# Optimization experiments

Measured on AMD Instinct MI355X. Metric: run time of the kernel, lower is better.

Reference implementation:

```python
import jax, jax.numpy as jnp
import numpy as np

B, S, D, H, L, V = 2, 1024, 512, 8, 4, 32000
DK = D // H
EPS = 1e-6


def _positional_encoding():
    # row i of the original (d_model, seq) array: sin if i even else cos of t/10000^(2i/D); transposed -> (S, D)
    i = jnp.arange(D, dtype=jnp.float32)
    ang = jnp.arange(S, dtype=jnp.float32)[:, None] / (10000.0 ** (2.0 * i / D))[None, :]
    return jnp.where((jnp.arange(D) % 2 == 0)[None, :], jnp.sin(ang), jnp.cos(ang))


def _layernorm(x, g, b):
    m = jnp.mean(x, axis=-1, keepdims=True)
    s = jnp.std(x, axis=-1, keepdims=True)
    return g / (s + EPS) * (x - m) + b


def _mha(x, wq, wk, wv, wo, mask):
    # wq/wk/wv: [H, D, DK]; all heads batched via einsum (equivalent to per-head loop + concat)
    q = jnp.einsum('bsd,hdk->bhsk', x, wq)
    k = jnp.einsum('bsd,hdk->bhsk', x, wk)
    v = jnp.einsum('bsd,hdk->bhsk', x, wv)
    scores = jnp.einsum('bhsk,bhtk->bhst', q, k) / np.float32(np.sqrt(DK))
    if mask is not None:
        scores = scores + mask  # additive upper-tri 1e-15, faithful to source
    attn = jax.nn.softmax(scores, axis=-1)
    o = jnp.einsum('bhst,bhtv->bhsv', attn, v)
    o = o.transpose(0, 2, 1, 3).reshape(B, S, D)  # concat heads
    return o @ wo


def setup_inputs() -> dict:
    key = jax.random.key(0)
    ks = jax.random.split(key, 13)
    n = lambda k, shape, s=0.05: jax.random.normal(k, shape, dtype=jnp.float32) * s
    return {
        'tokens': jax.random.randint(ks[0], (B, S), 0, V),
        'emb': n(ks[1], (V, D)),
        'Wq': n(ks[2], (L, 2, H, D, DK)),
        'Wk': n(ks[3], (L, 2, H, D, DK)),
        'Wv': n(ks[4], (L, 2, H, D, DK)),
        'Wo': n(ks[5], (L, 2, D, D)),
        'ln_gain': 1.0 + n(ks[6], (L, 3, S, D)),
        'ln_bias': n(ks[7], (L, 3, S, D)),
        'ffn_w1': n(ks[8], (L, D, D)),
        'ffn_b1': n(ks[9], (L, D)),
        'ffn_w2': n(ks[10], (L, D, D)),
        'ffn_b2': n(ks[11], (L, D)),
    }


def reference(tokens, emb, Wq, Wk, Wv, Wo, ln_gain, ln_bias, ffn_w1, ffn_b1, ffn_w2, ffn_b2):
    pe = _positional_encoding()
    # NOTE: source applies sqrt(d_model) scalar AFTER adding positional encoding
    x = (emb[tokens] + pe[None, :, :]) * np.float32(np.sqrt(D))
    # source 'mask' adds 1e-15 to strictly-upper triangle (effectively a no-op; kept faithful)
    mask = (jnp.triu(jnp.ones((S, S), dtype=jnp.float32), 1) * 1e-15)[None, None, :, :]
    for l in range(L):
        h = _mha(x, Wq[l, 0], Wk[l, 0], Wv[l, 0], Wo[l, 0], mask)
        x = _layernorm(x + h, ln_gain[l, 0], ln_bias[l, 0])
        h = _mha(x, Wq[l, 1], Wk[l, 1], Wv[l, 1], Wo[l, 1], None)
        x = _layernorm(x + h, ln_gain[l, 1], ln_bias[l, 1])
        h = jax.nn.relu(x @ ffn_w1[l] + ffn_b1[l]) @ ffn_w2[l] + ffn_b2[l]
        x = _layernorm(x + h, ln_gain[l, 2], ln_bias[l, 2])
    # tied output projection with softmax (SharedWeights on transposed embedding)
    return jax.nn.softmax(x @ emb.T, axis=-1)
```

## Files before the change

kernel.cpp:

```cpp
#include <hip/hip_runtime.h>
#include <hip/hip_bf16.h>

typedef unsigned short u16;
typedef short bf16x8 __attribute__((ext_vector_type(8)));
typedef float f32x4 __attribute__((ext_vector_type(4)));
typedef unsigned short u16x8 __attribute__((ext_vector_type(8)));

constexpr int kB = 2;
constexpr int kS = 1024;
constexpr int kD = 512;
constexpr int kH = 8;
constexpr int kDK = 64;
constexpr int kL = 4;
constexpr int kV = 32000;
constexpr int kM = kB * kS;
constexpr int kNB = kV / 128;

__device__ __forceinline__ u16 f2bh(float x) {
  unsigned u = __builtin_bit_cast(unsigned, x);
  unsigned r = u + 0x7fffu + ((u >> 16) & 1u);
  return (u16)(r >> 16);
}
__device__ __forceinline__ float bh2f(u16 h) {
  return __builtin_bit_cast(float, (unsigned)h << 16);
}
__device__ __forceinline__ void gload16(const u16* g, u16* l) {
  __builtin_amdgcn_global_load_lds(
      (const __attribute__((address_space(1))) unsigned int*)g,
      (__attribute__((address_space(3))) unsigned int*)l, 16, 0, 0);
}
__device__ __forceinline__ size_t swz_idx(int row, int k) {
  return (size_t)row * kD + (k & ~63) + ((((k >> 3) & 7) ^ (row & 7)) << 3) + (k & 7);
}

__global__ __launch_bounds__(256)
void conv_qkv(const float* __restrict__ Wq, const float* __restrict__ Wk,
              const float* __restrict__ Wv, u16* __restrict__ oh, u16* __restrict__ ol) {
  __shared__ float ld[64][65];
  const int kc = blockIdx.x, h = blockIdx.y, z = blockIdx.z;
  const int mat = z >> 3, lj = z & 7;
  const float* src = (mat == 0 ? Wq : mat == 1 ? Wk : Wv) +
                     ((size_t)(lj * kH + h)) * kD * kDK + (size_t)kc * 64 * kDK;
  const int t = threadIdx.x;
#pragma unroll
  for (int i = 0; i < 16; ++i) {
    const int idx = i * 256 + t;
    ld[idx >> 6][idx & 63] = src[idx];
  }
  __syncthreads();
  const int dkr = t >> 2, jb = t & 3;
  const size_t rowbase = ((size_t)lj * 1536 + mat * kD + h * kDK + dkr) * kD + kc * 64;
#pragma unroll
  for (int q = 0; q < 2; ++q) {
    const int jj = jb + q * 4;
    const int jsw = jj ^ (dkr & 7);
    u16x8 hi, lo;
#pragma unroll
    for (int e = 0; e < 8; ++e) {
      float v = ld[jj * 8 + e][dkr];
      hi[e] = f2bh(v);
      lo[e] = f2bh(v - bh2f(hi[e]));
    }
    *(u16x8*)&oh[rowbase + jsw * 8] = hi;
    *(u16x8*)&ol[rowbase + jsw * 8] = lo;
  }
}

__global__ __launch_bounds__(256)
void conv_sq(const float* __restrict__ Wo, const float* __restrict__ w1,
             const float* __restrict__ w2, u16* __restrict__ woh, u16* __restrict__ wol,
             u16* __restrict__ w1h, u16* __restrict__ w1l,
             u16* __restrict__ w2h, u16* __restrict__ w2l) {
  __shared__ float ld[64][65];
  const int kc = blockIdx.x, nc = blockIdx.y, mid = blockIdx.z;
  const float* src;
  u16 *dh, *dl;
  if (mid < 8) { src = Wo + (size_t)mid * kD * kD; dh = woh + (size_t)mid * kD * kD; dl = wol + (size_t)mid * kD * kD; }
  else if (mid < 12) { int l = mid - 8; src = w1 + (size_t)l * kD * kD; dh = w1h + (size_t)l * kD * kD; dl = w1l + (size_t)l * kD * kD; }
  else { int l = mid - 12; src = w2 + (size_t)l * kD * kD; dh = w2h + (size_t)l * kD * kD; dl = w2l + (size_t)l * kD * kD; }
  const int t = threadIdx.x;
#pragma unroll
  for (int i = 0; i < 16; ++i) {
    const int idx = i * 256 + t;
    const int kl = idx >> 6, nl = idx & 63;
    ld[kl][nl] = src[(size_t)(kc * 64 + kl) * kD + nc * 64 + nl];
  }
  __syncthreads();
  const int nr = t >> 2, jb = t & 3;
  const size_t rowbase = (size_t)(nc * 64 + nr) * kD + kc * 64;
#pragma unroll
  for (int q = 0; q < 2; ++q) {
    const int jj = jb + q * 4;
    const int jsw = jj ^ (nr & 7);
    u16x8 hi, lo;
#pragma unroll
    for (int e = 0; e < 8; ++e) {
      float v = ld[jj * 8 + e][nr];
      hi[e] = f2bh(v);
      lo[e] = f2bh(v - bh2f(hi[e]));
    }
    *(u16x8*)&dh[rowbase + jsw * 8] = hi;
    *(u16x8*)&dl[rowbase + jsw * 8] = lo;
  }
}

__global__ __launch_bounds__(256)
void conv_emb(const float* __restrict__ emb, u16* __restrict__ oh) {
  const int chunk = blockIdx.x * 256 + threadIdx.x;
  const int n = chunk >> 6, j = chunk & 63;
  const float* s = &emb[(size_t)n * kD + j * 8];
  float4 a = *(const float4*)s, b = *(const float4*)(s + 4);
  u16x8 hi;
  hi[0] = f2bh(a.x); hi[1] = f2bh(a.y); hi[2] = f2bh(a.z); hi[3] = f2bh(a.w);
  hi[4] = f2bh(b.x); hi[5] = f2bh(b.y); hi[6] = f2bh(b.z); hi[7] = f2bh(b.w);
  *(u16x8*)&oh[(size_t)n * kD + (j & ~7) * 8 + (((j & 7) ^ (n & 7)) << 3)] = hi;
}

__global__ __launch_bounds__(256)
void embed_kernel(const int* __restrict__ tokens, const float* __restrict__ emb,
                  float* __restrict__ x, u16* __restrict__ xh, u16* __restrict__ xl) {
  const int row = blockIdx.x;
  const int s = row & (kS - 1);
  const int tok = tokens[row];
  const float scl = sqrtf((float)kD);
  for (int d = threadIdx.x; d < kD; d += 256) {
    float e = emb[(size_t)tok * kD + d];
    float den = powf(10000.0f, 2.0f * (float)d / (float)kD);
    float ang = (float)s / den;
    float pe = ((d & 1) == 0) ? sinf(ang) : cosf(ang);
    float o = (e + pe) * scl;
    x[(size_t)row * kD + d] = o;
    u16 hi = f2bh(o);
    size_t p = swz_idx(row, d);
    xh[p] = hi;
    xl[p] = f2bh(o - bh2f(hi));
  }
}

template <int SPLIT, int BM, int BN, int OUT, int BIAS, int RELU>
__global__ __launch_bounds__(256)
void mgemm2(const u16* __restrict__ Ah, const u16* __restrict__ Al,
            const u16* __restrict__ Bh, const u16* __restrict__ Bl,
            float* __restrict__ Cf, u16* __restrict__ Ch, u16* __restrict__ Cl,
            const float* __restrict__ bias, float* __restrict__ partials,
            int Kd, int Nd) {
  static_assert(BM == BN, "");
  constexpr int MF = BM / 32, NF = BN / 32;
  constexpr int TA = BM * 64;
  constexpr int NT = (SPLIT == 3 ? 4 : 2);
  constexpr int BUF = NT * TA;
  __shared__ __align__(16) u16 lds[2 * BUF];
  __shared__ float plds[OUT == 3 ? 2 * BM : 1];
  const int t = threadIdx.x;
  const int lane = t & 63, g = lane >> 4, li = lane & 15;
  const int w = t >> 6, wr = w >> 1, wc = w & 1;
  const int m0 = blockIdx.x * BM, n0 = blockIdx.y * BN;

  f32x4 acc[MF][NF];
#pragma unroll
  for (int i = 0; i < MF; ++i)
#pragma unroll
    for (int j = 0; j < NF; ++j) acc[i][j] = (f32x4){0.f, 0.f, 0.f, 0.f};

  auto stage = [&](int c, int k0) {
    u16* base = &lds[c * BUF];
#pragma unroll
    for (int it = 0; it < BM / 32; ++it) {
      const int idx = it * 256 + t;
      const int r = idx >> 3, j = (idx & 7) * 8;
      gload16(&Ah[(size_t)(m0 + r) * Kd + k0 + j], &base[idx * 8]);
      if (SPLIT == 3)
        gload16(&Al[(size_t)(m0 + r) * Kd + k0 + j], &base[TA + idx * 8]);
      gload16(&Bh[(size_t)(n0 + r) * Kd + k0 + j],
              &base[(SPLIT == 3 ? 2 : 1) * TA + idx * 8]);
      if (SPLIT == 3)
        gload16(&Bl[(size_t)(n0 + r) * Kd + k0 + j], &base[3 * TA + idx * 8]);
    }
  };
  auto compute = [&](int c) {
    const u16* base = &lds[c * BUF];
#pragma unroll
    for (int s = 0; s < 2; ++s) {
      const int s4g = s * 4 + g;
      bf16x8 fah[MF], fbh[NF], fal[SPLIT == 3 ? MF : 1], fbl[SPLIT == 3 ? NF : 1];
#pragma unroll
      for (int fm = 0; fm < MF; ++fm) {
        const int row = wr * (BM / 2) + fm * 16 + li;
        const int off = row * 64 + ((s4g ^ (row & 7)) << 3);
        fah[fm] = *(const bf16x8*)&base[off];
        if (SPLIT == 3) fal[fm] = *(const bf16x8*)&base[TA + off];
      }
#pragma unroll
      for (int fn = 0; fn < NF; ++fn) {
        const int row = wc * (BN / 2) + fn * 16 + li;
        const int off = row * 64 + ((s4g ^ (row & 7)) << 3);
        fbh[fn] = *(const bf16x8*)&base[(SPLIT == 3 ? 2 : 1) * TA + off];
        if (SPLIT == 3) fbl[fn] = *(const bf16x8*)&base[3 * TA + off];
      }
#pragma unroll
      for (int fm = 0; fm < MF; ++fm)
#pragma unroll
        for (int fn = 0; fn < NF; ++fn) {
          acc[fm][fn] = __builtin_amdgcn_mfma_f32_16x16x32_bf16(
              fah[fm], fbh[fn], acc[fm][fn], 0, 0, 0);
          if (SPLIT == 3) {
            acc[fm][fn] = __builtin_amdgcn_mfma_f32_16x16x32_bf16(
                fal[fm], fbh[fn], acc[fm][fn], 0, 0, 0);
            acc[fm][fn] = __builtin_amdgcn_mfma_f32_16x16x32_bf16(
                fah[fm], fbl[fn], acc[fm][fn], 0, 0, 0);
          }
        }
    }
  };

  stage(0, 0);
  __syncthreads();
  int cur = 0;
  for (int k0 = 64; k0 < Kd; k0 += 64) {
    stage(cur ^ 1, k0);
    compute(cur);
    __syncthreads();
    cur ^= 1;
  }
  compute(cur);

#pragma unroll
  for (int fm = 0; fm < MF; ++fm)
#pragma unroll
    for (int fn = 0; fn < NF; ++fn)
#pragma unroll
      for (int r = 0; r < 4; ++r) {
        const int m = m0 + wr * (BM / 2) + fm * 16 + g * 4 + r;
        const int n = n0 + wc * (BN / 2) + fn * 16 + li;
        float c = acc[fm][fn][r];
        if (BIAS) c += bias[n];
        if (RELU) c = fmaxf(c, 0.0f);
        if (OUT == 0) {
          Cf[(size_t)m * Nd + n] = c;
        } else if (OUT == 1) {
          u16 hi = f2bh(c);
          size_t p = swz_idx(m, n);
          Ch[p] = hi;
          Cl[p] = f2bh(c - bh2f(hi));
        } else if (OUT == 2) {
          const int mat = n >> 9, h = (n >> 6) & 7, dk = n & 63;
          const int b_ = m >> 10, s_ = m & (kS - 1);
          Ch[(size_t)mat * ((size_t)kM * kDK * kH / 8) * 8 +
             (((size_t)(b_ * kH + h) * kS + s_) * kDK + dk)] = f2bh(c);
        } else {
          u16 q = f2bh(__expf(c));
          Ch[(size_t)m * Nd + n] = q;
          acc[fm][fn][r] = bh2f(q);
        }
      }
  if (OUT == 3) {
#pragma unroll
    for (int fm = 0; fm < MF; ++fm)
#pragma unroll
      for (int r = 0; r < 4; ++r) {
        float sv = 0.f;
#pragma unroll
        for (int fn = 0; fn < NF; ++fn) sv += acc[fm][fn][r];
        sv += __shfl_xor(sv, 1); sv += __shfl_xor(sv, 2);
        sv += __shfl_xor(sv, 4); sv += __shfl_xor(sv, 8);
        if (li == 0) plds[wc * BM + wr * (BM / 2) + fm * 16 + g * 4 + r] = sv;
      }
    __syncthreads();
    if (t < BM)
      partials[(size_t)(m0 + t) * gridDim.y + blockIdx.y] = plds[t] + plds[BM + t];
  }
}

__global__ __launch_bounds__(256)
void attn_kernel(const u16* __restrict__ qg, const u16* __restrict__ kg,
                 const u16* __restrict__ vg, u16* __restrict__ aoh,
                 u16* __restrict__ aol) {
  __shared__ __align__(16) u16 Kt[2][64][40];
  __shared__ __align__(16) u16 Vt[2][64][40];
  __shared__ __align__(16) u16 Pt[2][64][40];
  const int t = threadIdx.x;
  const int lane = t & 63;
  const int g = lane >> 4, li = lane & 15;
  const int w = t >> 6;
  const int bh = blockIdx.y;
  const int q0 = blockIdx.x * 64;
  const size_t base = (size_t)bh * kS * kDK;
  {
    const int r = t >> 2, dq = (t & 3) * 16;
    const u16* src = &qg[base + (size_t)(q0 + r) * kDK + dq];
    u16x8 a = *(const u16x8*)src;
    u16x8 b = *(const u16x8*)(src + 8);
    *(u16x8*)&Kt[dq >> 5][r][dq & 31] = a;
    *(u16x8*)&Kt[dq >> 5][r][(dq & 31) + 8] = b;
  }
  __syncthreads();
  bf16x8 qf0 = *(const bf16x8*)&Kt[0][w * 16 + li][g * 8];
  bf16x8 qf1 = *(const bf16x8*)&Kt[1][w * 16 + li][g * 8];

  float m_[4] = {-1e30f, -1e30f, -1e30f, -1e30f};
  float l_[4] = {0.f, 0.f, 0.f, 0.f};
  f32x4 apv[4];
#pragma unroll
  for (int i = 0; i < 4; ++i) apv[i] = (f32x4){0.f, 0.f, 0.f, 0.f};

  for (int kt = 0; kt < kS / 64; ++kt) {
    __syncthreads();
    {
      const int r = t >> 2, dq = (t & 3) * 16;
      const u16* ks = &kg[base + (size_t)(kt * 64 + r) * kDK + dq];
      u16x8 a = *(const u16x8*)ks;
      u16x8 b = *(const u16x8*)(ks + 8);
      *(u16x8*)&Kt[dq >> 5][r][dq & 31] = a;
      *(u16x8*)&Kt[dq >> 5][r][(dq & 31) + 8] = b;
      const u16* vs = &vg[base + (size_t)(kt * 64 + r) * kDK + dq];
      u16x8 va = *(const u16x8*)vs;
      u16x8 vb = *(const u16x8*)(vs + 8);
      const int vc = r >> 5, ko = (r & 31) >> 3, kp = r & 7;
#pragma unroll
      for (int i = 0; i < 8; ++i) {
        const int d = dq + i;
        Vt[vc][d][((ko ^ (d >> 4)) << 3) | kp] = va[i];
      }
#pragma unroll
      for (int i = 0; i < 8; ++i) {
        const int d = dq + 8 + i;
        Vt[vc][d][((ko ^ (d >> 4)) << 3) | kp] = vb[i];
      }
    }
    __syncthreads();
    f32x4 s[4];
#pragma unroll
    for (int nf = 0; nf < 4; ++nf) {
      bf16x8 k0 = *(const bf16x8*)&Kt[0][nf * 16 + li][g * 8];
      bf16x8 k1 = *(const bf16x8*)&Kt[1][nf * 16 + li][g * 8];
      f32x4 sa = (f32x4){0.f, 0.f, 0.f, 0.f};
      sa = __builtin_amdgcn_mfma_f32_16x16x32_bf16(qf0, k0, sa, 0, 0, 0);
      sa = __builtin_amdgcn_mfma_f32_16x16x32_bf16(qf1, k1, sa, 0, 0, 0);
      s[nf] = sa;
    }
    float corr[4];
#pragma unroll
    for (int r = 0; r < 4; ++r) {
      float tm = fmaxf(fmaxf(s[0][r], s[1][r]), fmaxf(s[2][r], s[3][r])) * 0.125f;
      tm = fmaxf(tm, __shfl_xor(tm, 1));
      tm = fmaxf(tm, __shfl_xor(tm, 2));
      tm = fmaxf(tm, __shfl_xor(tm, 4));
      tm = fmaxf(tm, __shfl_xor(tm, 8));
      const float nm = fmaxf(m_[r], tm);
      corr[r] = __expf(m_[r] - nm);
      m_[r] = nm;
    }
    float tsum[4] = {0.f, 0.f, 0.f, 0.f};
    u16 pb[4][4];
#pragma unroll
    for (int nf = 0; nf < 4; ++nf)
#pragma unroll
      for (int r = 0; r < 4; ++r) {
        float p = __expf(s[nf][r] * 0.125f - m_[r]);
        tsum[r] += p;
        pb[nf][r] = f2bh(p);
      }
#pragma unroll
    for (int r = 0; r < 4; ++r) {
      float ts = tsum[r];
      ts += __shfl_xor(ts, 1); ts += __shfl_xor(ts, 2);
      ts += __shfl_xor(ts, 4); ts += __shfl_xor(ts, 8);
      l_[r] = l_[r] * corr[r] + ts;
#pragma unroll
      for (int nf = 0; nf < 4; ++nf) apv[nf][r] *= corr[r];
    }
#pragma unroll
    for (int nf = 0; nf < 4; ++nf)
#pragma unroll
      for (int r = 0; r < 4; ++r)
        Pt[nf >> 1][w * 16 + g * 4 + r][(nf & 1) * 16 + li] = pb[nf][r];
    bf16x8 p0 = *(const bf16x8*)&Pt[0][w * 16 + li][g * 8];
    bf16x8 p1 = *(const bf16x8*)&Pt[1][w * 16 + li][g * 8];
#pragma unroll
    for (int nf = 0; nf < 4; ++nf) {
      bf16x8 v0 = *(const bf16x8*)&Vt[0][nf * 16 + li][((g ^ nf) & 3) * 8];
      bf16x8 v1 = *(const bf16x8*)&Vt[1][nf * 16 + li][((g ^ nf) & 3) * 8];
      apv[nf] = __builtin_amdgcn_mfma_f32_16x16x32_bf16(p0, v0, apv[nf], 0, 0, 0);
      apv[nf] = __builtin_amdgcn_mfma_f32_16x16x32_bf16(p1, v1, apv[nf], 0, 0, 0);
    }
  }
  const int b_ = bh >> 3, h_ = bh & 7;
#pragma unroll
  for (int r = 0; r < 4; ++r) {
    const float inv = 1.0f / l_[r];
    const int row = q0 + w * 16 + g * 4 + r;
    const int m = b_ * kS + row;
#pragma unroll
    for (int nf = 0; nf < 4; ++nf) {
      const int d = h_ * kDK + nf * 16 + li;
      float o = apv[nf][r] * inv;
      u16 hi = f2bh(o);
      size_t p = swz_idx(m, d);
      aoh[p] = hi;
      aol[p] = f2bh(o - bh2f(hi));
    }
  }
}

__global__ __launch_bounds__(256)
void ln_kernel(float* __restrict__ x, const float* __restrict__ h,
               const float* __restrict__ gain, const float* __restrict__ bias,
               u16* __restrict__ xh, u16* __restrict__ xl) {
  const int row = blockIdx.x;
  const int s = row & (kS - 1);
  const int t = threadIdx.x;
  float* xr = x + (size_t)row * kD;
  const float* hr = h + (size_t)row * kD;
  const float v0 = xr[t] + hr[t];
  const float v1 = xr[t + 256] + hr[t + 256];
  float sum = v0 + v1;
  float sq = v0 * v0 + v1 * v1;
#pragma unroll
  for (int off = 1; off < 64; off <<= 1) {
    sum += __shfl_xor(sum, off);
    sq += __shfl_xor(sq, off);
  }
  __shared__ float rs[4], rq[4];
  if ((t & 63) == 0) { rs[t >> 6] = sum; rq[t >> 6] = sq; }
  __syncthreads();
  sum = rs[0] + rs[1] + rs[2] + rs[3];
  sq = rq[0] + rq[1] + rq[2] + rq[3];
  const float mean = sum * (1.0f / kD);
  const float var = fmaxf(sq * (1.0f / kD) - mean * mean, 0.0f);
  const float inv = 1.0f / (sqrtf(var) + 1e-6f);
  const float* gr = gain + (size_t)s * kD;
  const float* br = bias + (size_t)s * kD;
  const float o0 = gr[t] * inv * (v0 - mean) + br[t];
  const float o1 = gr[t + 256] * inv * (v1 - mean) + br[t + 256];
  xr[t] = o0;
  xr[t + 256] = o1;
  {
    u16 hi = f2bh(o0);
    size_t p = swz_idx(row, t);
    xh[p] = hi; xl[p] = f2bh(o0 - bh2f(hi));
  }
  {
    u16 hi = f2bh(o1);
    size_t p = swz_idx(row, t + 256);
    xh[p] = hi; xl[p] = f2bh(o1 - bh2f(hi));
  }
}

__global__ __launch_bounds__(256)
void scale_kernel(const u16* __restrict__ expb, const float* __restrict__ partials,
                  float* __restrict__ out) {
  const int row = blockIdx.x;
  const int t = threadIdx.x;
  float s = (t < kNB) ? partials[(size_t)row * kNB + t] : 0.f;
#pragma unroll
  for (int off = 1; off < 64; off <<= 1) s += __shfl_xor(s, off);
  __shared__ float red[4];
  if ((t & 63) == 0) red[t >> 6] = s;
  __syncthreads();
  const float inv = 1.0f / (red[0] + red[1] + red[2] + red[3]);
  const u16x8* src = (const u16x8*)(expb + (size_t)row * kV);
  float4* dst = (float4*)(out + (size_t)row * kV);
  for (int i = t; i < kV / 8; i += 256) {
    u16x8 v = src[i];
    float4 a = make_float4(bh2f(v[0]) * inv, bh2f(v[1]) * inv,
                           bh2f(v[2]) * inv, bh2f(v[3]) * inv);
    float4 b = make_float4(bh2f(v[4]) * inv, bh2f(v[5]) * inv,
                           bh2f(v[6]) * inv, bh2f(v[7]) * inv);
    dst[i * 2] = a;
    dst[i * 2 + 1] = b;
  }
}

extern "C" void kernel_launch(void* const* d_in, const int* in_sizes, int n_in,
                              void* d_out, int out_size, void* d_ws, size_t ws_size,
                              hipStream_t stream) {
  (void)in_sizes; (void)n_in; (void)out_size; (void)ws_size;
  const int* tokens = (const int*)d_in[0];
  const float* emb = (const float*)d_in[1];
  const float* Wq = (const float*)d_in[2];
  const float* Wk = (const float*)d_in[3];
  const float* Wv = (const float*)d_in[4];
  const float* Wo = (const float*)d_in[5];
  const float* lng = (const float*)d_in[6];
  const float* lnb = (const float*)d_in[7];
  const float* w1 = (const float*)d_in[8];
  const float* b1 = (const float*)d_in[9];
  const float* w2 = (const float*)d_in[10];
  const float* b2 = (const float*)d_in[11];

  size_t off = 0;
  auto alloc = [&](size_t bytes) {
    void* p = (char*)d_ws + off;
    off += (bytes + 255) & ~(size_t)255;
    return p;
  };
  const size_t NA = (size_t)kM * kD;
  float* x = (float*)alloc(NA * 4);
  u16* xh = (u16*)alloc(NA * 2);
  u16* xl = (u16*)alloc(NA * 2);
  u16* qkvb = (u16*)alloc(3 * NA * 2);
  u16* aoh = (u16*)alloc(NA * 2);
  u16* aol = (u16*)alloc(NA * 2);
  float* t1 = (float*)alloc(NA * 4);
  u16* t1h = (u16*)alloc(NA * 2);
  u16* t1l = (u16*)alloc(NA * 2);
  float* ao2 = (float*)alloc(NA * 4);
  float* partials = (float*)alloc((size_t)kM * kNB * 4);
  u16* expb = (u16*)alloc((size_t)kM * kV * 2);
  u16* wqkvh = (u16*)alloc((size_t)8 * 1536 * kD * 2);
  u16* wqkvl = (u16*)alloc((size_t)8 * 1536 * kD * 2);
  u16* woh = (u16*)alloc((size_t)8 * kD * kD * 2);
  u16* wol = (u16*)alloc((size_t)8 * kD * kD * 2);
  u16* w1h = (u16*)alloc((size_t)4 * kD * kD * 2);
  u16* w1l = (u16*)alloc((size_t)4 * kD * kD * 2);
  u16* w2h = (u16*)alloc((size_t)4 * kD * kD * 2);
  u16* w2l = (u16*)alloc((size_t)4 * kD * kD * 2);
  u16* embh = (u16*)alloc((size_t)kV * kD * 2);

  conv_qkv<<<dim3(8, 8, 24), 256, 0, stream>>>(Wq, Wk, Wv, wqkvh, wqkvl);
  conv_sq<<<dim3(8, 8, 16), 256, 0, stream>>>(Wo, w1, w2, woh, wol, w1h, w1l, w2h, w2l);
  conv_emb<<<kV * kD / 8 / 256, 256, 0, stream>>>(emb, embh);
  embed_kernel<<<kM, 256, 0, stream>>>(tokens, emb, x, xh, xl);

  for (int l = 0; l < kL; ++l) {
    for (int j = 0; j < 2; ++j) {
      const size_t lj = (size_t)(l * 2 + j);
      mgemm2<3, 128, 128, 2, 0, 0><<<dim3(kM / 128, 12), 256, 0, stream>>>(
          xh, xl, wqkvh + lj * 1536 * kD, wqkvl + lj * 1536 * kD,
          nullptr, qkvb, nullptr, nullptr, nullptr, kD, 1536);
      attn_kernel<<<dim3(kS / 64, kB * kH), 256, 0, stream>>>(
          qkvb, qkvb + NA, qkvb + 2 * NA, aoh, aol);
      mgemm2<3, 64, 64, 0, 0, 0><<<dim3(kM / 64, kD / 64), 256, 0, stream>>>(
          aoh, aol, woh + lj * kD * kD, wol + lj * kD * kD,
          t1, nullptr, nullptr, nullptr, nullptr, kD, kD);
      ln_kernel<<<kM, 256, 0, stream>>>(x, t1, lng + (size_t)(l * 3 + j) * kS * kD,
                                        lnb + (size_t)(l * 3 + j) * kS * kD, xh, xl);
    }
    mgemm2<3, 64, 64, 1, 1, 1><<<dim3(kM / 64, kD / 64), 256, 0, stream>>>(
        xh, xl, w1h + (size_t)l * kD * kD, w1l + (size_t)l * kD * kD,
        nullptr, t1h, t1l, b1 + (size_t)l * kD, nullptr, kD, kD);
    mgemm2<3, 64, 64, 0, 1, 0><<<dim3(kM / 64, kD / 64), 256, 0, stream>>>(
        t1h, t1l, w2h + (size_t)l * kD * kD, w2l + (size_t)l * kD * kD,
        ao2, nullptr, nullptr, b2 + (size_t)l * kD, nullptr, kD, kD);
    ln_kernel<<<kM, 256, 0, stream>>>(x, ao2, lng + (size_t)(l * 3 + 2) * kS * kD,
                                      lnb + (size_t)(l * 3 + 2) * kS * kD, xh, xl);
  }
  mgemm2<1, 128, 128, 3, 0, 0><<<dim3(kM / 128, kNB), 256, 0, stream>>>(
      xh, nullptr, embh, nullptr, nullptr, expb, nullptr, nullptr, partials,
      kD, kV);
  scale_kernel<<<kM, 256, 0, stream>>>(expb, partials, (float*)d_out);
}
```

Measured before the change: 823.0 us.

## Replace split-bf16 three-pass GEMMs with single-pass fp16 and double-buffer attention K/V

Every layer GEMM previously split operands into bf16 hi/lo pairs and issued three MFMAs per tile to emulate fp32 accuracy. This switches all operands to a single fp16 representation with one MFMA per tile, which drops the lo buffers and cuts MFMA work and memory traffic roughly threefold. The attention kernel also moves to fp16 and double-buffers K/V tiles in LDS, prefetching the next tile into registers during compute. The cost is lower precision: fp16 has a narrower range, which is risky for activations scaled by sqrt(D), and the output error grows.

```diff
diff --git a/kernel.cpp b/kernel.cpp
--- a/kernel.cpp
+++ b/kernel.cpp
@@ -2,7 +2,7 @@
 #include <hip/hip_bf16.h>
 
 typedef unsigned short u16;
-typedef short bf16x8 __attribute__((ext_vector_type(8)));
+typedef _Float16 f16x8 __attribute__((ext_vector_type(8)));
 typedef float f32x4 __attribute__((ext_vector_type(4)));
 typedef unsigned short u16x8 __attribute__((ext_vector_type(8)));
 
@@ -16,6 +16,13 @@
 constexpr int kM = kB * kS;
 constexpr int kNB = kV / 128;
 
+__device__ __forceinline__ u16 f2fh(float x) {
+  _Float16 h = (_Float16)x;
+  return __builtin_bit_cast(u16, h);
+}
+__device__ __forceinline__ float fh2f(u16 h) {
+  return (float)__builtin_bit_cast(_Float16, h);
+}
 __device__ __forceinline__ u16 f2bh(float x) {
   unsigned u = __builtin_bit_cast(unsigned, x);
   unsigned r = u + 0x7fffu + ((u >> 16) & 1u);
@@ -35,7 +42,7 @@
 
 __global__ __launch_bounds__(256)
 void conv_qkv(const float* __restrict__ Wq, const float* __restrict__ Wk,
-              const float* __restrict__ Wv, u16* __restrict__ oh, u16* __restrict__ ol) {
+              const float* __restrict__ Wv, u16* __restrict__ oh) {
   __shared__ float ld[64][65];
   const int kc = blockIdx.x, h = blockIdx.y, z = blockIdx.z;
   const int mat = z >> 3, lj = z & 7;
@@ -54,30 +61,24 @@
   for (int q = 0; q < 2; ++q) {
     const int jj = jb + q * 4;
     const int jsw = jj ^ (dkr & 7);
-    u16x8 hi, lo;
-#pragma unroll
-    for (int e = 0; e < 8; ++e) {
-      float v = ld[jj * 8 + e][dkr];
-      hi[e] = f2bh(v);
-      lo[e] = f2bh(v - bh2f(hi[e]));
-    }
+    u16x8 hi;
+#pragma unroll
+    for (int e = 0; e < 8; ++e) hi[e] = f2fh(ld[jj * 8 + e][dkr]);
     *(u16x8*)&oh[rowbase + jsw * 8] = hi;
-    *(u16x8*)&ol[rowbase + jsw * 8] = lo;
   }
 }
 
 __global__ __launch_bounds__(256)
 void conv_sq(const float* __restrict__ Wo, const float* __restrict__ w1,
-             const float* __restrict__ w2, u16* __restrict__ woh, u16* __restrict__ wol,
-             u16* __restrict__ w1h, u16* __restrict__ w1l,
-             u16* __restrict__ w2h, u16* __restrict__ w2l) {
+             const float* __restrict__ w2, u16* __restrict__ woh,
+             u16* __restrict__ w1h, u16* __restrict__ w2h) {
   __shared__ float ld[64][65];
   const int kc = blockIdx.x, nc = blockIdx.y, mid = blockIdx.z;
   const float* src;
-  u16 *dh, *dl;
-  if (mid < 8) { src = Wo + (size_t)mid * kD * kD; dh = woh + (size_t)mid * kD * kD; dl = wol + (size_t)mid * kD * kD; }
-  else if (mid < 12) { int l = mid - 8; src = w1 + (size_t)l * kD * kD; dh = w1h + (size_t)l * kD * kD; dl = w1l + (size_t)l * kD * kD; }
-  else { int l = mid - 12; src = w2 + (size_t)l * kD * kD; dh = w2h + (size_t)l * kD * kD; dl = w2l + (size_t)l * kD * kD; }
+  u16* dh;
+  if (mid < 8) { src = Wo + (size_t)mid * kD * kD; dh = woh + (size_t)mid * kD * kD; }
+  else if (mid < 12) { int l = mid - 8; src = w1 + (size_t)l * kD * kD; dh = w1h + (size_t)l * kD * kD; }
+  else { int l = mid - 12; src = w2 + (size_t)l * kD * kD; dh = w2h + (size_t)l * kD * kD; }
   const int t = threadIdx.x;
 #pragma unroll
   for (int i = 0; i < 16; ++i) {
@@ -92,15 +93,10 @@
   for (int q = 0; q < 2; ++q) {
     const int jj = jb + q * 4;
     const int jsw = jj ^ (nr & 7);
-    u16x8 hi, lo;
-#pragma unroll
-    for (int e = 0; e < 8; ++e) {
-      float v = ld[jj * 8 + e][nr];
-      hi[e] = f2bh(v);
-      lo[e] = f2bh(v - bh2f(hi[e]));
-    }
+    u16x8 hi;
+#pragma unroll
+    for (int e = 0; e < 8; ++e) hi[e] = f2fh(ld[jj * 8 + e][nr]);
     *(u16x8*)&dh[rowbase + jsw * 8] = hi;
-    *(u16x8*)&dl[rowbase + jsw * 8] = lo;
   }
 }
 
@@ -111,14 +107,14 @@
   const float* s = &emb[(size_t)n * kD + j * 8];
   float4 a = *(const float4*)s, b = *(const float4*)(s + 4);
   u16x8 hi;
-  hi[0] = f2bh(a.x); hi[1] = f2bh(a.y); hi[2] = f2bh(a.z); hi[3] = f2bh(a.w);
-  hi[4] = f2bh(b.x); hi[5] = f2bh(b.y); hi[6] = f2bh(b.z); hi[7] = f2bh(b.w);
+  hi[0] = f2fh(a.x); hi[1] = f2fh(a.y); hi[2] = f2fh(a.z); hi[3] = f2fh(a.w);
+  hi[4] = f2fh(b.x); hi[5] = f2fh(b.y); hi[6] = f2fh(b.z); hi[7] = f2fh(b.w);
   *(u16x8*)&oh[(size_t)n * kD + (j & ~7) * 8 + (((j & 7) ^ (n & 7)) << 3)] = hi;
 }
 
 __global__ __launch_bounds__(256)
 void embed_kernel(const int* __restrict__ tokens, const float* __restrict__ emb,
-                  float* __restrict__ x, u16* __restrict__ xh, u16* __restrict__ xl) {
+                  float* __restrict__ x, u16* __restrict__ xh) {
   const int row = blockIdx.x;
   const int s = row & (kS - 1);
   const int tok = tokens[row];
@@ -130,25 +126,20 @@
     float pe = ((d & 1) == 0) ? sinf(ang) : cosf(ang);
     float o = (e + pe) * scl;
     x[(size_t)row * kD + d] = o;
-    u16 hi = f2bh(o);
-    size_t p = swz_idx(row, d);
-    xh[p] = hi;
-    xl[p] = f2bh(o - bh2f(hi));
-  }
-}
-
-template <int SPLIT, int BM, int BN, int OUT, int BIAS, int RELU>
-__global__ __launch_bounds__(256)
-void mgemm2(const u16* __restrict__ Ah, const u16* __restrict__ Al,
-            const u16* __restrict__ Bh, const u16* __restrict__ Bl,
-            float* __restrict__ Cf, u16* __restrict__ Ch, u16* __restrict__ Cl,
+    xh[swz_idx(row, d)] = f2fh(o);
+  }
+}
+
+template <int BM, int BN, int OUT, int BIAS, int RELU>
+__global__ __launch_bounds__(256)
+void mgemm2(const u16* __restrict__ Ah, const u16* __restrict__ Bh,
+            float* __restrict__ Cf, u16* __restrict__ Ch,
             const float* __restrict__ bias, float* __restrict__ partials,
             int Kd, int Nd) {
   static_assert(BM == BN, "");
   constexpr int MF = BM / 32, NF = BN / 32;
   constexpr int TA = BM * 64;
-  constexpr int NT = (SPLIT == 3 ? 4 : 2);
-  constexpr int BUF = NT * TA;
+  constexpr int BUF = 2 * TA;
   __shared__ __align__(16) u16 lds[2 * BUF];
   __shared__ float plds[OUT == 3 ? 2 * BM : 1];
   const int t = threadIdx.x;
@@ -169,12 +160,7 @@
       const int idx = it * 256 + t;
       const int r = idx >> 3, j = (idx & 7) * 8;
       gload16(&Ah[(size_t)(m0 + r) * Kd + k0 + j], &base[idx * 8]);
-      if (SPLIT == 3)
-        gload16(&Al[(size_t)(m0 + r) * Kd + k0 + j], &base[TA + idx * 8]);
-      gload16(&Bh[(size_t)(n0 + r) * Kd + k0 + j],
-              &base[(SPLIT == 3 ? 2 : 1) * TA + idx * 8]);
-      if (SPLIT == 3)
-        gload16(&Bl[(size_t)(n0 + r) * Kd + k0 + j], &base[3 * TA + idx * 8]);
+      gload16(&Bh[(size_t)(n0 + r) * Kd + k0 + j], &base[TA + idx * 8]);
     }
   };
   auto compute = [&](int c) {
@@ -182,34 +168,23 @@
 #pragma unroll
     for (int s = 0; s < 2; ++s) {
       const int s4g = s * 4 + g;
-      bf16x8 fah[MF], fbh[NF], fal[SPLIT == 3 ? MF : 1], fbl[SPLIT == 3 ? NF : 1];
+      f16x8 fah[MF], fbh[NF];
 #pragma unroll
       for (int fm = 0; fm < MF; ++fm) {
         const int row = wr * (BM / 2) + fm * 16 + li;
-        const int off = row * 64 + ((s4g ^ (row & 7)) << 3);
-        fah[fm] = *(const bf16x8*)&base[off];
-        if (SPLIT == 3) fal[fm] = *(const bf16x8*)&base[TA + off];
+        fah[fm] = *(const f16x8*)&base[row * 64 + ((s4g ^ (row & 7)) << 3)];
       }
 #pragma unroll
       for (int fn = 0; fn < NF; ++fn) {
         const int row = wc * (BN / 2) + fn * 16 + li;
-        const int off = row * 64 + ((s4g ^ (row & 7)) << 3);
-        fbh[fn] = *(const bf16x8*)&base[(SPLIT == 3 ? 2 : 1) * TA + off];
-        if (SPLIT == 3) fbl[fn] = *(const bf16x8*)&base[3 * TA + off];
+        fbh[fn] = *(const f16x8*)&base[TA + row * 64 + ((s4g ^ (row & 7)) << 3)];
       }
 #pragma unroll
       for (int fm = 0; fm < MF; ++fm)
 #pragma unroll
-        for (int fn = 0; fn < NF; ++fn) {
-          acc[fm][fn] = __builtin_amdgcn_mfma_f32_16x16x32_bf16(
+        for (int fn = 0; fn < NF; ++fn)
+          acc[fm][fn] = __builtin_amdgcn_mfma_f32_16x16x32_f16(
               fah[fm], fbh[fn], acc[fm][fn], 0, 0, 0);
-          if (SPLIT == 3) {
-            acc[fm][fn] = __builtin_amdgcn_mfma_f32_16x16x32_bf16(
-                fal[fm], fbh[fn], acc[fm][fn], 0, 0, 0);
-            acc[fm][fn] = __builtin_amdgcn_mfma_f32_16x16x32_bf16(
-                fah[fm], fbl[fn], acc[fm][fn], 0, 0, 0);
-          }
-        }
     }
   };
 
@@ -238,15 +213,12 @@
         if (OUT == 0) {
           Cf[(size_t)m * Nd + n] = c;
         } else if (OUT == 1) {
-          u16 hi = f2bh(c);
-          size_t p = swz_idx(m, n);
-          Ch[p] = hi;
-          Cl[p] = f2bh(c - bh2f(hi));
+          Ch[swz_idx(m, n)] = f2fh(c);
         } else if (OUT == 2) {
           const int mat = n >> 9, h = (n >> 6) & 7, dk = n & 63;
           const int b_ = m >> 10, s_ = m & (kS - 1);
-          Ch[(size_t)mat * ((size_t)kM * kDK * kH / 8) * 8 +
-             (((size_t)(b_ * kH + h) * kS + s_) * kDK + dk)] = f2bh(c);
+          Ch[((size_t)mat * kM) * kD +
+             (((size_t)(b_ * kH + h) * kS + s_) * kDK + dk)] = f2fh(c);
         } else {
           u16 q = f2bh(__expf(c));
           Ch[(size_t)m * Nd + n] = q;
@@ -273,10 +245,9 @@
 
 __global__ __launch_bounds__(256)
 void attn_kernel(const u16* __restrict__ qg, const u16* __restrict__ kg,
-                 const u16* __restrict__ vg, u16* __restrict__ aoh,
-                 u16* __restrict__ aol) {
-  __shared__ __align__(16) u16 Kt[2][64][40];
-  __shared__ __align__(16) u16 Vt[2][64][40];
+                 const u16* __restrict__ vg, u16* __restrict__ aoh) {
+  __shared__ __align__(16) u16 Kt[2][2][64][40];
+  __shared__ __align__(16) u16 Vt[2][2][64][40];
   __shared__ __align__(16) u16 Pt[2][64][40];
   const int t = threadIdx.x;
   const int lane = t & 63;
@@ -285,17 +256,19 @@
   const int bh = blockIdx.y;
   const int q0 = blockIdx.x * 64;
   const size_t base = (size_t)bh * kS * kDK;
+  const int r = t >> 2, dq = (t & 3) * 16;
+
   {
-    const int r = t >> 2, dq = (t & 3) * 16;
     const u16* src = &qg[base + (size_t)(q0 + r) * kDK + dq];
     u16x8 a = *(const u16x8*)src;
     u16x8 b = *(const u16x8*)(src + 8);
-    *(u16x8*)&Kt[dq >> 5][r][dq & 31] = a;
-    *(u16x8*)&Kt[dq >> 5][r][(dq & 31) + 8] = b;
-  }
-  __syncthreads();
-  bf16x8 qf0 = *(const bf16x8*)&Kt[0][w * 16 + li][g * 8];
-  bf16x8 qf1 = *(const bf16x8*)&Kt[1][w * 16 + li][g * 8];
+    *(u16x8*)&Pt[dq >> 5][r][dq & 31] = a;
+    *(u16x8*)&Pt[dq >> 5][r][(dq & 31) + 8] = b;
+  }
+  __syncthreads();
+  f16x8 qf0 = *(const f16x8*)&Pt[0][w * 16 + li][g * 8];
+  f16x8 qf1 = *(const f16x8*)&Pt[1][w * 16 + li][g * 8];
+  __syncthreads();
 
   float m_[4] = {-1e30f, -1e30f, -1e30f, -1e30f};
   float l_[4] = {0.f, 0.f, 0.f, 0.f};
@@ -303,101 +276,104 @@
 #pragma unroll
   for (int i = 0; i < 4; ++i) apv[i] = (f32x4){0.f, 0.f, 0.f, 0.f};
 
+  u16x8 ka, kb, va, vb;
+  auto load_tile = [&](int kt) {
+    const u16* ks = &kg[base + (size_t)(kt * 64 + r) * kDK + dq];
+    ka = *(const u16x8*)ks;
+    kb = *(const u16x8*)(ks + 8);
+    const u16* vs = &vg[base + (size_t)(kt * 64 + r) * kDK + dq];
+    va = *(const u16x8*)vs;
+    vb = *(const u16x8*)(vs + 8);
+  };
+  auto store_tile = [&](int c) {
+    *(u16x8*)&Kt[c][dq >> 5][r][dq & 31] = ka;
+    *(u16x8*)&Kt[c][dq >> 5][r][(dq & 31) + 8] = kb;
+    const int vc = r >> 5, ko = (r & 31) >> 3, kp = r & 7;
+#pragma unroll
+    for (int i = 0; i < 8; ++i) {
+      const int d = dq + i;
+      Vt[c][vc][d][((ko ^ (d >> 4)) << 3) | kp] = va[i];
+    }
+#pragma unroll
+    for (int i = 0; i < 8; ++i) {
+      const int d = dq + 8 + i;
+      Vt[c][vc][d][((ko ^ (d >> 4)) << 3) | kp] = vb[i];
+    }
+  };
+
+  load_tile(0);
+  store_tile(0);
   for (int kt = 0; kt < kS / 64; ++kt) {
-    __syncthreads();
-    {
-      const int r = t >> 2, dq = (t & 3) * 16;
-      const u16* ks = &kg[base + (size_t)(kt * 64 + r) * kDK + dq];
-      u16x8 a = *(const u16x8*)ks;
-      u16x8 b = *(const u16x8*)(ks + 8);
-      *(u16x8*)&Kt[dq >> 5][r][dq & 31] = a;
-      *(u16x8*)&Kt[dq >> 5][r][(dq & 31) + 8] = b;
-      const u16* vs = &vg[base + (size_t)(kt * 64 + r) * kDK + dq];
-      u16x8 va = *(const u16x8*)vs;
-      u16x8 vb = *(const u16x8*)(vs + 8);
-      const int vc = r >> 5, ko = (r & 31) >> 3, kp = r & 7;
-#pragma unroll
-      for (int i = 0; i < 8; ++i) {
-        const int d = dq + i;
-        Vt[vc][d][((ko ^ (d >> 4)) << 3) | kp] = va[i];
-      }
-#pragma unroll
-      for (int i = 0; i < 8; ++i) {
-        const int d = dq + 8 + i;
-        Vt[vc][d][((ko ^ (d >> 4)) << 3) | kp] = vb[i];
-      }
-    }
+    const int c = kt & 1;
+    if (kt < kS / 64 - 1) load_tile(kt + 1);
     __syncthreads();
     f32x4 s[4];
 #pragma unroll
     for (int nf = 0; nf < 4; ++nf) {
-      bf16x8 k0 = *(const bf16x8*)&Kt[0][nf * 16 + li][g * 8];
-      bf16x8 k1 = *(const bf16x8*)&Kt[1][nf * 16 + li][g * 8];
+      f16x8 k0 = *(const f16x8*)&Kt[c][0][nf * 16 + li][g * 8];
+      f16x8 k1 = *(const f16x8*)&Kt[c][1][nf * 16 + li][g * 8];
       f32x4 sa = (f32x4){0.f, 0.f, 0.f, 0.f};
-      sa = __builtin_amdgcn_mfma_f32_16x16x32_bf16(qf0, k0, sa, 0, 0, 0);
-      sa = __builtin_amdgcn_mfma_f32_16x16x32_bf16(qf1, k1, sa, 0, 0, 0);
+      sa = __builtin_amdgcn_mfma_f32_16x16x32_f16(qf0, k0, sa, 0, 0, 0);
+      sa = __builtin_amdgcn_mfma_f32_16x16x32_f16(qf1, k1, sa, 0, 0, 0);
       s[nf] = sa;
     }
     float corr[4];
 #pragma unroll
-    for (int r = 0; r < 4; ++r) {
-      float tm = fmaxf(fmaxf(s[0][r], s[1][r]), fmaxf(s[2][r], s[3][r])) * 0.125f;
+    for (int rr = 0; rr < 4; ++rr) {
+      float tm = fmaxf(fmaxf(s[0][rr], s[1][rr]), fmaxf(s[2][rr], s[3][rr])) * 0.125f;
       tm = fmaxf(tm, __shfl_xor(tm, 1));
       tm = fmaxf(tm, __shfl_xor(tm, 2));
       tm = fmaxf(tm, __shfl_xor(tm, 4));
       tm = fmaxf(tm, __shfl_xor(tm, 8));
-      const float nm = fmaxf(m_[r], tm);
-      corr[r] = __expf(m_[r] - nm);
-      m_[r] = nm;
+      const float nm = fmaxf(m_[rr], tm);
+      corr[rr] = __expf(m_[rr] - nm);
+      m_[rr] = nm;
     }
     float tsum[4] = {0.f, 0.f, 0.f, 0.f};
     u16 pb[4][4];
 #pragma unroll
     for (int nf = 0; nf < 4; ++nf)
 #pragma unroll
-      for (int r = 0; r < 4; ++r) {
-        float p = __expf(s[nf][r] * 0.125f - m_[r]);
-        tsum[r] += p;
-        pb[nf][r] = f2bh(p);
+      for (int rr = 0; rr < 4; ++rr) {
+        float p = __expf(s[nf][rr] * 0.125f - m_[rr]);
+        tsum[rr] += p;
+        pb[nf][rr] = f2fh(p);
       }
 #pragma unroll
-    for (int r = 0; r < 4; ++r) {
-      float ts = tsum[r];
+    for (int rr = 0; rr < 4; ++rr) {
+      float ts = tsum[rr];
       ts += __shfl_xor(ts, 1); ts += __shfl_xor(ts, 2);
       ts += __shfl_xor(ts, 4); ts += __shfl_xor(ts, 8);
-      l_[r] = l_[r] * corr[r] + ts;
-#pragma unroll
-      for (int nf = 0; nf < 4; ++nf) apv[nf][r] *= corr[r];
+      l_[rr] = l_[rr] * corr[rr] + ts;
+#pragma unroll
+      for (int nf = 0; nf < 4; ++nf) apv[nf][rr] *= corr[rr];
     }
 #pragma unroll
     for (int nf = 0; nf < 4; ++nf)
 #pragma unroll
-      for (int r = 0; r < 4; ++r)
-        Pt[nf >> 1][w * 16 + g * 4 + r][(nf & 1) * 16 + li] = pb[nf][r];
-    bf16x8 p0 = *(const bf16x8*)&Pt[0][w * 16 + li][g * 8];
-    bf16x8 p1 = *(const bf16x8*)&Pt[1][w * 16 + li][g * 8];
+      for (int rr = 0; rr < 4; ++rr)
+        Pt[nf >> 1][w * 16 + g * 4 + rr][(nf & 1) * 16 + li] = pb[nf][rr];
+    f16x8 p0 = *(const f16x8*)&Pt[0][w * 16 + li][g * 8];
+    f16x8 p1 = *(const f16x8*)&Pt[1][w * 16 + li][g * 8];
 #pragma unroll
     for (int nf = 0; nf < 4; ++nf) {
-      bf16x8 v0 = *(const bf16x8*)&Vt[0][nf * 16 + li][((g ^ nf) & 3) * 8];
-      bf16x8 v1 = *(const bf16x8*)&Vt[1][nf * 16 + li][((g ^ nf) & 3) * 8];
-      apv[nf] = __builtin_amdgcn_mfma_f32_16x16x32_bf16(p0, v0, apv[nf], 0, 0, 0);
-      apv[nf] = __builtin_amdgcn_mfma_f32_16x16x32_bf16(p1, v1, apv[nf], 0, 0, 0);
-    }
+      f16x8 v0 = *(const f16x8*)&Vt[c][0][nf * 16 + li][((g ^ nf) & 3) * 8];
+      f16x8 v1 = *(const f16x8*)&Vt[c][1][nf * 16 + li][((g ^ nf) & 3) * 8];
+      apv[nf] = __builtin_amdgcn_mfma_f32_16x16x32_f16(p0, v0, apv[nf], 0, 0, 0);
+      apv[nf] = __builtin_amdgcn_mfma_f32_16x16x32_f16(p1, v1, apv[nf], 0, 0, 0);
+    }
+    if (kt < kS / 64 - 1) store_tile(c ^ 1);
   }
   const int b_ = bh >> 3, h_ = bh & 7;
 #pragma unroll
-  for (int r = 0; r < 4; ++r) {
-    const float inv = 1.0f / l_[r];
-    const int row = q0 + w * 16 + g * 4 + r;
+  for (int rr = 0; rr < 4; ++rr) {
+    const float inv = 1.0f / l_[rr];
+    const int row = q0 + w * 16 + g * 4 + rr;
     const int m = b_ * kS + row;
 #pragma unroll
     for (int nf = 0; nf < 4; ++nf) {
       const int d = h_ * kDK + nf * 16 + li;
-      float o = apv[nf][r] * inv;
-      u16 hi = f2bh(o);
-      size_t p = swz_idx(m, d);
-      aoh[p] = hi;
-      aol[p] = f2bh(o - bh2f(hi));
+      aoh[swz_idx(m, d)] = f2fh(apv[nf][rr] * inv);
     }
   }
 }
@@ -405,7 +381,7 @@
 __global__ __launch_bounds__(256)
 void ln_kernel(float* __restrict__ x, const float* __restrict__ h,
                const float* __restrict__ gain, const float* __restrict__ bias,
-               u16* __restrict__ xh, u16* __restrict__ xl) {
+               u16* __restrict__ xh) {
   const int row = blockIdx.x;
   const int s = row & (kS - 1);
   const int t = threadIdx.x;
@@ -434,16 +410,8 @@
   const float o1 = gr[t + 256] * inv * (v1 - mean) + br[t + 256];
   xr[t] = o0;
   xr[t + 256] = o1;
-  {
-    u16 hi = f2bh(o0);
-    size_t p = swz_idx(row, t);
-    xh[p] = hi; xl[p] = f2bh(o0 - bh2f(hi));
-  }
-  {
-    u16 hi = f2bh(o1);
-    size_t p = swz_idx(row, t + 256);
-    xh[p] = hi; xl[p] = f2bh(o1 - bh2f(hi));
-  }
+  xh[swz_idx(row, t)] = f2fh(o0);
+  xh[swz_idx(row, t + 256)] = f2fh(o1);
 }
 
 __global__ __launch_bounds__(256)
@@ -497,56 +465,46 @@
   const size_t NA = (size_t)kM * kD;
   float* x = (float*)alloc(NA * 4);
   u16* xh = (u16*)alloc(NA * 2);
-  u16* xl = (u16*)alloc(NA * 2);
   u16* qkvb = (u16*)alloc(3 * NA * 2);
   u16* aoh = (u16*)alloc(NA * 2);
-  u16* aol = (u16*)alloc(NA * 2);
   float* t1 = (float*)alloc(NA * 4);
   u16* t1h = (u16*)alloc(NA * 2);
-  u16* t1l = (u16*)alloc(NA * 2);
   float* ao2 = (float*)alloc(NA * 4);
   float* partials = (float*)alloc((size_t)kM * kNB * 4);
   u16* expb = (u16*)alloc((size_t)kM * kV * 2);
   u16* wqkvh = (u16*)alloc((size_t)8 * 1536 * kD * 2);
-  u16* wqkvl = (u16*)alloc((size_t)8 * 1536 * kD * 2);
   u16* woh = (u16*)alloc((size_t)8 * kD * kD * 2);
-  u16* wol = (u16*)alloc((size_t)8 * kD * kD * 2);
   u16* w1h = (u16*)alloc((size_t)4 * kD * kD * 2);
-  u16* w1l = (u16*)alloc((size_t)4 * kD * kD * 2);
   u16* w2h = (u16*)alloc((size_t)4 * kD * kD * 2);
-  u16* w2l = (u16*)alloc((size_t)4 * kD * kD * 2);
   u16* embh = (u16*)alloc((size_t)kV * kD * 2);
 
-  conv_qkv<<<dim3(8, 8, 24), 256, 0, stream>>>(Wq, Wk, Wv, wqkvh, wqkvl);
-  conv_sq<<<dim3(8, 8, 16), 256, 0, stream>>>(Wo, w1, w2, woh, wol, w1h, w1l, w2h, w2l);
+  conv_qkv<<<dim3(8, 8, 24), 256, 0, stream>>>(Wq, Wk, Wv, wqkvh);
+  conv_sq<<<dim3(8, 8, 16), 256, 0, stream>>>(Wo, w1, w2, woh, w1h, w2h);
   conv_emb<<<kV * kD / 8 / 256, 256, 0, stream>>>(emb, embh);
-  embed_kernel<<<kM, 256, 0, stream>>>(tokens, emb, x, xh, xl);
+  embed_kernel<<<kM, 256, 0, stream>>>(tokens, emb, x, xh);
 
   for (int l = 0; l < kL; ++l) {
     for (int j = 0; j < 2; ++j) {
       const size_t lj = (size_t)(l * 2 + j);
-      mgemm2<3, 128, 128, 2, 0, 0><<<dim3(kM / 128, 12), 256, 0, stream>>>(
-          xh, xl, wqkvh + lj * 1536 * kD, wqkvl + lj * 1536 * kD,
-          nullptr, qkvb, nullptr, nullptr, nullptr, kD, 1536);
+      mgemm2<128, 128, 2, 0, 0><<<dim3(kM / 128, 12), 256, 0, stream>>>(
+          xh, wqkvh + lj * 1536 * kD, nullptr, qkvb, nullptr, nullptr, kD, 1536);
       attn_kernel<<<dim3(kS / 64, kB * kH), 256, 0, stream>>>(
-          qkvb, qkvb + NA, qkvb + 2 * NA, aoh, aol);
-      mgemm2<3, 64, 64, 0, 0, 0><<<dim3(kM / 64, kD / 64), 256, 0, stream>>>(
-          aoh, aol, woh + lj * kD * kD, wol + lj * kD * kD,
-          t1, nullptr, nullptr, nullptr, nullptr, kD, kD);
+          qkvb, qkvb + NA, qkvb + 2 * NA, aoh);
+      mgemm2<64, 64, 0, 0, 0><<<dim3(kM / 64, kD / 64), 256, 0, stream>>>(
+          aoh, woh + lj * kD * kD, t1, nullptr, nullptr, nullptr, kD, kD);
       ln_kernel<<<kM, 256, 0, stream>>>(x, t1, lng + (size_t)(l * 3 + j) * kS * kD,
-                                        lnb + (size_t)(l * 3 + j) * kS * kD, xh, xl);
-    }
-    mgemm2<3, 64, 64, 1, 1, 1><<<dim3(kM / 64, kD / 64), 256, 0, stream>>>(
-        xh, xl, w1h + (size_t)l * kD * kD, w1l + (size_t)l * kD * kD,
-        nullptr, t1h, t1l, b1 + (size_t)l * kD, nullptr, kD, kD);
-    mgemm2<3, 64, 64, 0, 1, 0><<<dim3(kM / 64, kD / 64), 256, 0, stream>>>(
-        t1h, t1l, w2h + (size_t)l * kD * kD, w2l + (size_t)l * kD * kD,
-        ao2, nullptr, nullptr, b2 + (size_t)l * kD, nullptr, kD, kD);
+                                        lnb + (size_t)(l * 3 + j) * kS * kD, xh);
+    }
+    mgemm2<64, 64, 1, 1, 1><<<dim3(kM / 64, kD / 64), 256, 0, stream>>>(
+        xh, w1h + (size_t)l * kD * kD, nullptr, t1h, b1 + (size_t)l * kD,
+        nullptr, kD, kD);
+    mgemm2<64, 64, 0, 1, 0><<<dim3(kM / 64, kD / 64), 256, 0, stream>>>(
+        t1h, w2h + (size_t)l * kD * kD, ao2, nullptr, b2 + (size_t)l * kD,
+        nullptr, kD, kD);
     ln_kernel<<<kM, 256, 0, stream>>>(x, ao2, lng + (size_t)(l * 3 + 2) * kS * kD,
-                                      lnb + (size_t)(l * 3 + 2) * kS * kD, xh, xl);
-  }
-  mgemm2<1, 128, 128, 3, 0, 0><<<dim3(kM / 128, kNB), 256, 0, stream>>>(
-      xh, nullptr, embh, nullptr, nullptr, expb, nullptr, nullptr, partials,
-      kD, kV);
+                                      lnb + (size_t)(l * 3 + 2) * kS * kD, xh);
+  }
+  mgemm2<128, 128, 3, 0, 0><<<dim3(kM / 128, kNB), 256, 0, stream>>>(
+      xh, embh, nullptr, expb, nullptr, partials, kD, kV);
   scale_kernel<<<kM, 256, 0, stream>>>(expb, partials, (float*)d_out);
 }
```

New measurement: 669.4 us. 1.23x faster.
